# Kernel tuning notes

Hardware: AMD Instinct MI355X
Metric: run time of the kernel (lower is better)

## Reference

```python
import jax, jax.numpy as jnp
import numpy as np

EMB = 1024
HEADS = 16
B, N = 2, 2048

def setup_inputs() -> dict:
    key = jax.random.key(0)
    ks = jax.random.split(key, 9)
    s = 1.0 / np.sqrt(EMB)
    return {
        "x": jax.random.normal(ks[0], (B, N, EMB), dtype=jnp.float32),
        "Wq": jax.random.normal(ks[1], (EMB, EMB), dtype=jnp.float32) * s,
        "bq": jax.random.normal(ks[2], (EMB,), dtype=jnp.float32) * 0.01,
        "Wk": jax.random.normal(ks[3], (EMB, EMB), dtype=jnp.float32) * s,
        "bk": jax.random.normal(ks[4], (EMB,), dtype=jnp.float32) * 0.01,
        "Wv": jax.random.normal(ks[5], (EMB, EMB), dtype=jnp.float32) * s,
        "bv": jax.random.normal(ks[6], (EMB,), dtype=jnp.float32) * 0.01,
        "Wo": jax.random.normal(ks[7], (EMB, EMB), dtype=jnp.float32) * s,
        "bo": jax.random.normal(ks[8], (EMB,), dtype=jnp.float32) * 0.01,
    }

def _split_heads(t):
    b, n, e = t.shape
    return t.reshape(b, n, HEADS, e // HEADS).transpose(0, 2, 1, 3)  # b h n d

def reference(x, Wq, bq, Wk, bk, Wv, bv, Wo, bo):
    q = _split_heads(x @ Wq + bq)
    k = _split_heads(x @ Wk + bk)
    v = _split_heads(x @ Wv + bv)
    # NOTE: original scales by sqrt(emb_size), not sqrt(head_dim)
    scaling = jnp.asarray(EMB, x.dtype) ** 0.5
    energy = jnp.einsum('bhqd,bhkd->bhqk', q, k)
    att = jax.nn.softmax(energy / scaling, axis=-1)
    out = jnp.einsum('bhqk,bhkd->bhqd', att, v)
    out = out.transpose(0, 2, 1, 3).reshape(x.shape[0], x.shape[1], EMB)
    return out @ Wo + bo
```

## Files before the change

kernel.cpp:

```cpp
#include <hip/hip_runtime.h>
#include <hip/hip_bf16.h>

typedef __bf16 bf16_t;
typedef bf16_t bf16x8 __attribute__((ext_vector_type(8)));
typedef float f32x4 __attribute__((ext_vector_type(4)));
typedef float f32x2 __attribute__((ext_vector_type(2)));
typedef float f32x16 __attribute__((ext_vector_type(16)));

#define EMB 1024
#define HEADS 16
#define BATCH 2
#define SEQ 2048
#define HD 64
#define TOKENS (BATCH * SEQ)

__device__ __forceinline__ void gld16(bf16_t* lds_dst, const bf16_t* g_src) {
    __builtin_amdgcn_global_load_lds(
        (const __attribute__((address_space(1))) unsigned int*)g_src,
        (__attribute__((address_space(3))) unsigned int*)lds_dst, 16, 0, 0);
}

__device__ __forceinline__ unsigned cvt_pk_bf16(float lo, float hi) {
    unsigned r;
    asm("v_cvt_pk_bf16_f32 %0, %1, %2" : "=v"(r) : "v"(lo), "v"(hi));
    return r;
}

__device__ __forceinline__ float exp2_fast(float x) {
#if __has_builtin(__builtin_amdgcn_exp2f)
    return __builtin_amdgcn_exp2f(x);
#else
    return __expf(x * 0.69314718056f);
#endif
}

#define WAITV(N) asm volatile("s_waitcnt vmcnt(" #N ")" ::: "memory")
#define BAR() __builtin_amdgcn_s_barrier()

__global__ __launch_bounds__(256) void prep_all(
    const float* __restrict__ x, bf16_t* __restrict__ xb,
    const float* __restrict__ W0, const float* __restrict__ W1,
    const float* __restrict__ W2, const float* __restrict__ W3,
    bf16_t* __restrict__ T0, bf16_t* __restrict__ T1,
    bf16_t* __restrict__ T2, bf16_t* __restrict__ T3) {
    __shared__ __align__(16) bf16_t T[64][72];
    if (blockIdx.x < 1024) {
        size_t i = ((size_t)blockIdx.x * 256 + threadIdx.x) * 16;
        f32x4 v0 = *(const f32x4*)&x[i];
        f32x4 v1 = *(const f32x4*)&x[i + 4];
        f32x4 v2 = *(const f32x4*)&x[i + 8];
        f32x4 v3 = *(const f32x4*)&x[i + 12];
        bf16x8 o0, o1;
#pragma unroll
        for (int j = 0; j < 4; ++j) {
            o0[j] = (bf16_t)v0[j]; o0[4 + j] = (bf16_t)v1[j];
            o1[j] = (bf16_t)v2[j]; o1[4 + j] = (bf16_t)v3[j];
        }
        *(bf16x8*)&xb[i] = o0;
        *(bf16x8*)&xb[i + 8] = o1;
        return;
    }
    int t = blockIdx.x - 1024;
    int z = t >> 8, rid = t & 255;
    const float* src = (z == 0) ? W0 : (z == 1) ? W1 : (z == 2) ? W2 : W3;
    bf16_t* dst = (z == 0) ? T0 : (z == 1) ? T1 : (z == 2) ? T2 : T3;
    int k0 = (rid >> 4) * 64, n0 = (rid & 15) * 64;
    int r = threadIdx.x >> 2, c4 = (threadIdx.x & 3) * 16;
    f32x4 v[4];
#pragma unroll
    for (int q = 0; q < 4; ++q)
        v[q] = *(const f32x4*)&src[(size_t)(k0 + r) * 1024 + n0 + c4 + q * 4];
#pragma unroll
    for (int j = 0; j < 16; ++j) T[c4 + j][r] = (bf16_t)v[j >> 2][j & 3];
    __syncthreads();
    bf16x8 o0 = *(const bf16x8*)&T[r][c4];
    bf16x8 o1 = *(const bf16x8*)&T[r][c4 + 8];
    *(bf16x8*)&dst[(size_t)(n0 + r) * 1024 + k0 + c4] = o0;
    *(bf16x8*)&dst[(size_t)(n0 + r) * 1024 + k0 + c4 + 8] = o1;
}

template <typename TO>
__global__ __launch_bounds__(512) void gemm256(
    const bf16_t* __restrict__ A, const bf16_t* __restrict__ W,
    const float* __restrict__ b0, const float* __restrict__ b1, const float* __restrict__ b2,
    TO* __restrict__ o0, TO* __restrict__ o1, TO* __restrict__ o2,
    int md0, int md1, int md2, float sc0, float sc1, float sc2,
    int MP, int CM, int CSH, int NP) {
    __shared__ __align__(16) bf16_t As[3][256 * 64];
    __shared__ __align__(16) bf16_t Bs[3][128 * 64];

    const int tid = threadIdx.x, w = tid >> 6, lane = tid & 63;
    const int quad = lane >> 4, c = lane & 15;
    const int wm = (w >> 1) * 64, wn = (w & 1) * 64;

    const int lin = blockIdx.x;
    const int xc = lin & 7, t = lin >> 3;
    const int mi = MP * (xc & CM) + (t % MP);
    const int ni = NP * (xc >> CSH) + (t / MP);
    const int m0 = mi * 256, n0 = ni * 128;

    const int z = n0 >> 10;
    const float* bias = (z == 0) ? b0 : (z == 1) ? b1 : b2;
    TO* out = (z == 0) ? o0 : (z == 1) ? o1 : o2;
    const int mode = (z == 0) ? md0 : (z == 1) ? md1 : md2;
    const float scale = (z == 0) ? sc0 : (z == 1) ? sc1 : sc2;
    const int nz = n0 & 1023;

    f32x4 acc[4][4];
#pragma unroll
    for (int i = 0; i < 4; ++i)
#pragma unroll
        for (int j = 0; j < 4; ++j) acc[i][j] = (f32x4){0.f, 0.f, 0.f, 0.f};

    const int r8 = lane >> 3, sg = lane & 7;
    const int g8 = (sg ^ r8) * 8;
    const bf16_t* Ag = A + (size_t)m0 * 1024;
    const bf16_t* Bg = W + (size_t)n0 * 1024;
    int gA[4], lA[4], gB[2], lB[2];
#pragma unroll
    for (int s = 0; s < 4; ++s) {
        lA[s] = (w * 32 + s * 8) * 64;
        gA[s] = (w * 32 + s * 8 + r8) * 1024 + g8;
    }
#pragma unroll
    for (int s = 0; s < 2; ++s) {
        lB[s] = (w * 16 + s * 8) * 64;
        gB[s] = (w * 16 + s * 8 + r8) * 1024 + g8;
    }

    const int so = (quad ^ (c & 7)) * 8;
    int rA[4], rB[4];
#pragma unroll
    for (int i = 0; i < 4; ++i) {
        rA[i] = (wm + i * 16 + c) * 64;
        rB[i] = (wn + i * 16 + c) * 64;
    }

#define STAGE(BUF, T)                                                          \
    {                                                                          \
        int kn = (T) * 64;                                                     \
        _Pragma("unroll")                                                      \
        for (int s = 0; s < 4; ++s) gld16(&As[BUF][lA[s]], &Ag[gA[s] + kn]);   \
        _Pragma("unroll")                                                      \
        for (int s = 0; s < 2; ++s) gld16(&Bs[BUF][lB[s]], &Bg[gB[s] + kn]);   \
    }

#define FRAGS(CUR)                                                             \
    {                                                                          \
        _Pragma("unroll")                                                      \
        for (int ks = 0; ks < 2; ++ks) {                                       \
            int sk = so ^ (ks << 5);                                           \
            bf16x8 af[4], bfv[4];                                              \
            _Pragma("unroll")                                                  \
            for (int i = 0; i < 4; ++i)                                        \
                af[i] = *(const bf16x8*)&As[CUR][rA[i] + sk];                  \
            _Pragma("unroll")                                                  \
            for (int i = 0; i < 4; ++i)                                        \
                bfv[i] = *(const bf16x8*)&Bs[CUR][rB[i] + sk];                 \
            __builtin_amdgcn_s_setprio(1);                                     \
            _Pragma("unroll")                                                  \
            for (int mt = 0; mt < 4; ++mt)                                     \
                _Pragma("unroll")                                              \
                for (int nt = 0; nt < 4; ++nt)                                 \
                    acc[mt][nt] = __builtin_amdgcn_mfma_f32_16x16x32_bf16(     \
                        af[mt], bfv[nt], acc[mt][nt], 0, 0, 0);                \
            __builtin_amdgcn_s_setprio(0);                                     \
        }                                                                      \
    }

#define GSTEP(T, CUR)                                                          \
    {                                                                          \
        WAITV(6);                                                              \
        BAR();                                                                 \
        STAGE(((CUR) + 2) % 3, (T) + 2)                                        \
        FRAGS(CUR)                                                             \
    }

    STAGE(0, 0)
    STAGE(1, 1)
    for (int T = 0; T < 12; T += 3) {
        GSTEP(T, 0)
        GSTEP(T + 1, 1)
        GSTEP(T + 2, 2)
    }
    GSTEP(12, 0)
    GSTEP(13, 1)
    WAITV(6); BAR(); FRAGS(2)
    WAITV(0); BAR(); FRAGS(0)
#undef GSTEP
#undef FRAGS
#undef STAGE

    typedef TO TOx4 __attribute__((ext_vector_type(4)));
#pragma unroll
    for (int nt = 0; nt < 4; ++nt) {
        int colz = nz + wn + nt * 16 + c;
        float bv = bias[colz];
#pragma unroll
        for (int mt = 0; mt < 4; ++mt) {
            if (mode == 2) {
                int row = m0 + wm + mt * 16 + quad * 4;
                int bb = row >> 11, n = row & 2047;
                int hh = colz >> 6, d = colz & 63;
                TOx4 pk;
#pragma unroll
                for (int r = 0; r < 4; ++r)
                    pk[r] = (TO)((acc[mt][nt][r] + bv) * scale);
                *(TOx4*)&out[((size_t)(bb * HEADS + hh) * HD + d) * SEQ + n] = pk;
            } else {
#pragma unroll
                for (int r = 0; r < 4; ++r) {
                    int row = m0 + wm + mt * 16 + quad * 4 + r;
                    float v = (acc[mt][nt][r] + bv) * scale;
                    size_t idx;
                    if (mode == 0) {
                        idx = (size_t)row * 1024 + colz;
                    } else {
                        int bb = row >> 11, n = row & 2047;
                        int hh = colz >> 6, d = colz & 63;
                        idx = ((size_t)(bb * HEADS + hh) * SEQ + n) * HD + d;
                    }
                    out[idx] = (TO)v;
                }
            }
        }
    }
}

__global__ __launch_bounds__(256) void attn_kernel(
    const bf16_t* __restrict__ Q, const bf16_t* __restrict__ K,
    const bf16_t* __restrict__ Vt, bf16_t* __restrict__ O) {
    __shared__ __align__(16) bf16_t Ks[3][64 * 64];
    __shared__ __align__(16) bf16_t Vs[3][64 * 64];

    const int tid = threadIdx.x, w = tid >> 6, lane = tid & 63;
    const int hi = lane >> 5, lq = lane & 31;

    const int lin = blockIdx.x + (blockIdx.y << 4);
    const int xcd = lin & 7, slot = lin >> 3;
    const int bh = xcd + ((slot >> 4) << 3);
    const int q0 = (slot & 15) << 7;
    const int b = bh >> 4, h = bh & 15;

    const int srow8 = lane >> 3, sch = lane & 7;

    const bf16_t* Kg0 = K + (size_t)bh * SEQ * HD;
    const bf16_t* Vg0 = Vt + (size_t)bh * HD * SEQ;

    int sl[2], sgK[2], sgV[2];
#pragma unroll
    for (int s = 0; s < 2; ++s) {
        int rg = (w * 2 + s) * 8;
        int row = rg + srow8;
        int g = sch ^ (row & 7);
        sl[s] = rg * 64;
        sgK[s] = row * 64 + g * 8;
        sgV[s] = row * SEQ + g * 8;
    }
    int rd[4];
#pragma unroll
    for (int dc = 0; dc < 4; ++dc)
        rd[dc] = lq * 64 + (((dc * 2 + hi) ^ (lq & 7)) * 8);

    bf16x8 qf[4];
    {
        const bf16_t* Qrow = Q + ((size_t)bh * SEQ + q0 + w * 32 + lq) * HD;
#pragma unroll
        for (int dc = 0; dc < 4; ++dc)
            qf[dc] = *(const bf16x8*)&Qrow[(dc * 2 + hi) * 8];
    }

#pragma unroll
    for (int s = 0; s < 2; ++s) {
        gld16(&Ks[0][sl[s]], &Kg0[sgK[s]]);
        gld16(&Vs[0][sl[s]], &Vg0[sgV[s]]);
    }
#pragma unroll
    for (int s = 0; s < 2; ++s) {
        gld16(&Ks[1][sl[s]], &Kg0[64 * HD + sgK[s]]);
        gld16(&Vs[1][sl[s]], &Vg0[64 + sgV[s]]);
    }

    f32x16 Zf;
#pragma unroll
    for (int r = 0; r < 16; ++r) Zf[r] = 0.f;

    f32x16 Oacc0, Oacc1;
#pragma unroll
    for (int r = 0; r < 16; ++r) { Oacc0[r] = 0.f; Oacc1[r] = 0.f; }
    f32x2 lpA = (f32x2){0.f, 0.f}, lpB = (f32x2){0.f, 0.f};

    const bf16_t* KgN = Kg0 + 2 * 64 * HD;
    const bf16_t* VgN = Vg0 + 2 * 64;

#define PACKFRAG(SS, c2, dstIdx)                                               \
        {                                                                      \
            unsigned pa = cvt_pk_bf16(SS[8 * (c2) + 0], SS[8 * (c2) + 1]);     \
            unsigned pb = cvt_pk_bf16(SS[8 * (c2) + 4], SS[8 * (c2) + 5]);     \
            unsigned pc = cvt_pk_bf16(SS[8 * (c2) + 2], SS[8 * (c2) + 3]);     \
            unsigned pd = cvt_pk_bf16(SS[8 * (c2) + 6], SS[8 * (c2) + 7]);     \
            asm volatile("v_permlane32_swap_b32 %0, %1" : "+v"(pa), "+v"(pb)); \
            asm volatile("v_permlane32_swap_b32 %0, %1" : "+v"(pc), "+v"(pd)); \
            union { unsigned u[4]; bf16x8 v; } pu;                             \
            pu.u[0] = pa; pu.u[1] = pc; pu.u[2] = pb; pu.u[3] = pd;            \
            pf[dstIdx] = pu.v;                                                 \
        }

#define ACORE(CUR)                                                             \
    {                                                                          \
        f32x16 St0, St1;                                                       \
        __builtin_amdgcn_s_setprio(1);                                         \
        {                                                                      \
            bf16x8 k0 = *(const bf16x8*)&Ks[CUR][rd[0]];                       \
            bf16x8 k1 = *(const bf16x8*)&Ks[CUR][rd[0] + 2048];                \
            St0 = __builtin_amdgcn_mfma_f32_32x32x16_bf16(k0, qf[0], Zf, 0, 0, 0); \
            St1 = __builtin_amdgcn_mfma_f32_32x32x16_bf16(k1, qf[0], Zf, 0, 0, 0); \
        }                                                                      \
        _Pragma("unroll")                                                      \
        for (int dc = 1; dc < 4; ++dc) {                                       \
            bf16x8 k0 = *(const bf16x8*)&Ks[CUR][rd[dc]];                      \
            bf16x8 k1 = *(const bf16x8*)&Ks[CUR][rd[dc] + 2048];               \
            St0 = __builtin_amdgcn_mfma_f32_32x32x16_bf16(k0, qf[dc], St0, 0, 0, 0); \
            St1 = __builtin_amdgcn_mfma_f32_32x32x16_bf16(k1, qf[dc], St1, 0, 0, 0); \
        }                                                                      \
        __builtin_amdgcn_s_setprio(0);                                         \
        _Pragma("unroll")                                                      \
        for (int r = 0; r < 16; r += 2) {                                      \
            St0[r] = exp2_fast(St0[r]); St0[r + 1] = exp2_fast(St0[r + 1]);    \
            lpA += (f32x2){St0[r], St0[r + 1]};                                \
            St1[r] = exp2_fast(St1[r]); St1[r + 1] = exp2_fast(St1[r + 1]);    \
            lpB += (f32x2){St1[r], St1[r + 1]};                                \
        }                                                                      \
        bf16x8 pf[4];                                                          \
        PACKFRAG(St0, 0, 0) PACKFRAG(St0, 1, 1)                                \
        PACKFRAG(St1, 0, 2) PACKFRAG(St1, 1, 3)                                \
        __builtin_amdgcn_s_setprio(1);                                         \
        _Pragma("unroll")                                                      \
        for (int f = 0; f < 4; ++f) {                                          \
            bf16x8 v0 = *(const bf16x8*)&Vs[CUR][rd[f]];                       \
            bf16x8 v1 = *(const bf16x8*)&Vs[CUR][rd[f] + 2048];                \
            Oacc0 = __builtin_amdgcn_mfma_f32_32x32x16_bf16(pf[f], v0, Oacc0, 0, 0, 0); \
            Oacc1 = __builtin_amdgcn_mfma_f32_32x32x16_bf16(pf[f], v1, Oacc1, 0, 0, 0); \
        }                                                                      \
        __builtin_amdgcn_s_setprio(0);                                         \
    }

#define ASTEP(CUR)                                                             \
    {                                                                          \
        WAITV(4);                                                              \
        BAR();                                                                 \
        _Pragma("unroll")                                                      \
        for (int s = 0; s < 2; ++s) {                                          \
            gld16(&Ks[((CUR) + 2) % 3][sl[s]], &KgN[sgK[s]]);                  \
            gld16(&Vs[((CUR) + 2) % 3][sl[s]], &VgN[sgV[s]]);                  \
        }                                                                      \
        KgN += 64 * HD; VgN += 64;                                             \
        ACORE(CUR)                                                             \
    }

    for (int t = 0; t < 30; t += 3) {
        ASTEP(0) ASTEP(1) ASTEP(2)
    }
    WAITV(4); BAR(); ACORE(0)
    WAITV(0); BAR(); ACORE(1)
#undef ASTEP
#undef ACORE
#undef PACKFRAG

    float lp = (lpA[0] + lpA[1]) + (lpB[0] + lpB[1]);
    lp += __shfl_xor(lp, 32);
    float rl = 1.0f / lp;

#pragma unroll
    for (int r = 0; r < 16; ++r) {
        int q_loc = (r & 3) + 8 * (r >> 2) + 4 * hi;
        float rr = __shfl(rl, q_loc);
        int qrow = q0 + w * 32 + q_loc;
        size_t base = ((size_t)(b * SEQ + qrow)) * EMB + h * 64;
        O[base + lq] = (bf16_t)(Oacc0[r] * rr);
        O[base + 32 + lq] = (bf16_t)(Oacc1[r] * rr);
    }
}

extern "C" void kernel_launch(void* const* d_in, const int* in_sizes, int n_in,
                              void* d_out, int out_size, void* d_ws, size_t ws_size,
                              hipStream_t stream) {
    (void)in_sizes; (void)n_in; (void)out_size; (void)ws_size;
    const float* x  = (const float*)d_in[0];
    const float* Wq = (const float*)d_in[1];
    const float* bq = (const float*)d_in[2];
    const float* Wk = (const float*)d_in[3];
    const float* bk = (const float*)d_in[4];
    const float* Wv = (const float*)d_in[5];
    const float* bv = (const float*)d_in[6];
    const float* Wo = (const float*)d_in[7];
    const float* bo = (const float*)d_in[8];

    bf16_t* ws = (bf16_t*)d_ws;
    const size_t NELEM = (size_t)TOKENS * EMB;
    const size_t WELEM = (size_t)EMB * EMB;
    bf16_t* Qb  = ws;
    bf16_t* Kb  = ws + NELEM;
    bf16_t* Vtb = ws + 2 * NELEM;
    bf16_t* Ob  = ws + 3 * NELEM;
    bf16_t* xb  = ws + 4 * NELEM;
    bf16_t* Wt0 = ws + 5 * NELEM;
    bf16_t* Wt1 = Wt0 + WELEM;
    bf16_t* Wt2 = Wt0 + 2 * WELEM;
    bf16_t* Wt3 = Wt0 + 3 * WELEM;
    (void)Wt1; (void)Wt2;

    hipLaunchKernelGGL(prep_all, dim3(2048), dim3(256), 0, stream,
                       x, xb, Wq, Wk, Wv, Wo, Wt0, Wt1, Wt2, Wt3);
    hipLaunchKernelGGL((gemm256<bf16_t>), dim3(384), dim3(512), 0, stream,
                       xb, Wt0, bq, bk, bv, Qb, Kb, Vtb,
                       1, 1, 2, 0.0450842204f, 1.0f, 1.0f,
                       4, 3, 2, 12);
    hipLaunchKernelGGL(attn_kernel, dim3(16, 32), dim3(256), 0, stream, Qb, Kb, Vtb, Ob);
    hipLaunchKernelGGL((gemm256<float>), dim3(128), dim3(512), 0, stream,
                       Ob, Wt3, bo, bo, bo,
                       (float*)d_out, (float*)d_out, (float*)d_out,
                       0, 0, 0, 1.0f, 1.0f, 1.0f,
                       2, 7, 3, 8);
}
```

Measured before the change: 202.7 us.

## Process 128-key tiles per step with double-buffered LDS in attention

The attention loop now handles two 64-key subtiles per iteration (128 keys) using double buffering instead of a 3-stage ring of 64-key tiles. This halves the number of barriers and waits per key and gives more independent MFMAs per phase, and launch bounds now request 2 blocks per SM. The cost is a shallower prefetch (one tile ahead, with a full wait vmcnt(0) before each barrier) and higher register pressure from four score accumulators and eight P fragments.

Result: faster. 198.0 us (-2.3%).

```diff
diff --git a/kernel.cpp b/kernel.cpp
--- a/kernel.cpp
+++ b/kernel.cpp
@@ -227,11 +227,11 @@
     }
 }
 
-__global__ __launch_bounds__(256) void attn_kernel(
+__global__ __launch_bounds__(256, 2) void attn_kernel(
     const bf16_t* __restrict__ Q, const bf16_t* __restrict__ K,
     const bf16_t* __restrict__ Vt, bf16_t* __restrict__ O) {
-    __shared__ __align__(16) bf16_t Ks[3][64 * 64];
-    __shared__ __align__(16) bf16_t Vs[3][64 * 64];
+    __shared__ __align__(16) bf16_t Ks[2][2 * 64 * 64];
+    __shared__ __align__(16) bf16_t Vs[2][2 * 64 * 64];
 
     const int tid = threadIdx.x, w = tid >> 6, lane = tid & 63;
     const int hi = lane >> 5, lq = lane & 31;
@@ -270,16 +270,20 @@
             qf[dc] = *(const bf16x8*)&Qrow[(dc * 2 + hi) * 8];
     }
 
-#pragma unroll
-    for (int s = 0; s < 2; ++s) {
-        gld16(&Ks[0][sl[s]], &Kg0[sgK[s]]);
-        gld16(&Vs[0][sl[s]], &Vg0[sgV[s]]);
-    }
-#pragma unroll
-    for (int s = 0; s < 2; ++s) {
-        gld16(&Ks[1][sl[s]], &Kg0[64 * HD + sgK[s]]);
-        gld16(&Vs[1][sl[s]], &Vg0[64 + sgV[s]]);
-    }
+#define STAGEPH(BUF, PH)                                                       \
+    {                                                                          \
+        const bf16_t* Kp = Kg0 + (size_t)(PH) * 128 * HD;                      \
+        const bf16_t* Vp = Vg0 + (PH) * 128;                                   \
+        _Pragma("unroll")                                                      \
+        for (int s = 0; s < 2; ++s) {                                          \
+            gld16(&Ks[BUF][sl[s]], &Kp[sgK[s]]);                               \
+            gld16(&Ks[BUF][4096 + sl[s]], &Kp[4096 + sgK[s]]);                 \
+            gld16(&Vs[BUF][sl[s]], &Vp[sgV[s]]);                               \
+            gld16(&Vs[BUF][4096 + sl[s]], &Vp[64 + sgV[s]]);                   \
+        }                                                                      \
+    }
+
+    STAGEPH(0, 0)
 
     f32x16 Zf;
 #pragma unroll
@@ -289,9 +293,6 @@
 #pragma unroll
     for (int r = 0; r < 16; ++r) { Oacc0[r] = 0.f; Oacc1[r] = 0.f; }
     f32x2 lpA = (f32x2){0.f, 0.f}, lpB = (f32x2){0.f, 0.f};
-
-    const bf16_t* KgN = Kg0 + 2 * 64 * HD;
-    const bf16_t* VgN = Vg0 + 2 * 64;
 
 #define PACKFRAG(SS, c2, dstIdx)                                               \
         {                                                                      \
@@ -306,66 +307,79 @@
             pf[dstIdx] = pu.v;                                                 \
         }
 
-#define ACORE(CUR)                                                             \
+#define MFMA32(A, B, C) __builtin_amdgcn_mfma_f32_32x32x16_bf16(A, B, C, 0, 0, 0)
+
+#define ACORE2(BUF)                                                            \
     {                                                                          \
-        f32x16 St0, St1;                                                       \
+        f32x16 SA0, SA1, SB0, SB1;                                             \
         __builtin_amdgcn_s_setprio(1);                                         \
         {                                                                      \
-            bf16x8 k0 = *(const bf16x8*)&Ks[CUR][rd[0]];                       \
-            bf16x8 k1 = *(const bf16x8*)&Ks[CUR][rd[0] + 2048];                \
-            St0 = __builtin_amdgcn_mfma_f32_32x32x16_bf16(k0, qf[0], Zf, 0, 0, 0); \
-            St1 = __builtin_amdgcn_mfma_f32_32x32x16_bf16(k1, qf[0], Zf, 0, 0, 0); \
+            bf16x8 a0 = *(const bf16x8*)&Ks[BUF][rd[0]];                       \
+            bf16x8 a1 = *(const bf16x8*)&Ks[BUF][rd[0] + 2048];                \
+            bf16x8 b0 = *(const bf16x8*)&Ks[BUF][rd[0] + 4096];                \
+            bf16x8 b1 = *(const bf16x8*)&Ks[BUF][rd[0] + 6144];                \
+            SA0 = MFMA32(a0, qf[0], Zf);                                       \
+            SA1 = MFMA32(a1, qf[0], Zf);                                       \
+            SB0 = MFMA32(b0, qf[0], Zf);                                       \
+            SB1 = MFMA32(b1, qf[0], Zf);                                       \
         }                                                                      \
         _Pragma("unroll")                                                      \
         for (int dc = 1; dc < 4; ++dc) {                                       \
-            bf16x8 k0 = *(const bf16x8*)&Ks[CUR][rd[dc]];                      \
-            bf16x8 k1 = *(const bf16x8*)&Ks[CUR][rd[dc] + 2048];               \
-            St0 = __builtin_amdgcn_mfma_f32_32x32x16_bf16(k0, qf[dc], St0, 0, 0, 0); \
-            St1 = __builtin_amdgcn_mfma_f32_32x32x16_bf16(k1, qf[dc], St1, 0, 0, 0); \
+            bf16x8 a0 = *(const bf16x8*)&Ks[BUF][rd[dc]];                      \
+            bf16x8 a1 = *(const bf16x8*)&Ks[BUF][rd[dc] + 2048];               \
+            bf16x8 b0 = *(const bf16x8*)&Ks[BUF][rd[dc] + 4096];               \
+            bf16x8 b1 = *(const bf16x8*)&Ks[BUF][rd[dc] + 6144];               \
+            SA0 = MFMA32(a0, qf[dc], SA0);                                     \
+            SA1 = MFMA32(a1, qf[dc], SA1);                                     \
+            SB0 = MFMA32(b0, qf[dc], SB0);                                     \
+            SB1 = MFMA32(b1, qf[dc], SB1);                                     \
         }                                                                      \
         __builtin_amdgcn_s_setprio(0);                                         \
         _Pragma("unroll")                                                      \
         for (int r = 0; r < 16; r += 2) {                                      \
-            St0[r] = exp2_fast(St0[r]); St0[r + 1] = exp2_fast(St0[r + 1]);    \
-            lpA += (f32x2){St0[r], St0[r + 1]};                                \
-            St1[r] = exp2_fast(St1[r]); St1[r + 1] = exp2_fast(St1[r + 1]);    \
-            lpB += (f32x2){St1[r], St1[r + 1]};                                \
-        }                                                                      \
-        bf16x8 pf[4];                                                          \
-        PACKFRAG(St0, 0, 0) PACKFRAG(St0, 1, 1)                                \
-        PACKFRAG(St1, 0, 2) PACKFRAG(St1, 1, 3)                                \
+            SA0[r] = exp2_fast(SA0[r]); SA0[r + 1] = exp2_fast(SA0[r + 1]);    \
+            lpA += (f32x2){SA0[r], SA0[r + 1]};                                \
+            SA1[r] = exp2_fast(SA1[r]); SA1[r + 1] = exp2_fast(SA1[r + 1]);    \
+            lpB += (f32x2){SA1[r], SA1[r + 1]};                                \
+            SB0[r] = exp2_fast(SB0[r]); SB0[r + 1] = exp2_fast(SB0[r + 1]);    \
+            lpA += (f32x2){SB0[r], SB0[r + 1]};                                \
+            SB1[r] = exp2_fast(SB1[r]); SB1[r + 1] = exp2_fast(SB1[r + 1]);    \
+            lpB += (f32x2){SB1[r], SB1[r + 1]};                                \
+        }                                                                      \
+        bf16x8 pf[8];                                                          \
+        PACKFRAG(SA0, 0, 0) PACKFRAG(SA0, 1, 1)                                \
+        PACKFRAG(SA1, 0, 2) PACKFRAG(SA1, 1, 3)                                \
+        PACKFRAG(SB0, 0, 4) PACKFRAG(SB0, 1, 5)                                \
+        PACKFRAG(SB1, 0, 6) PACKFRAG(SB1, 1, 7)                                \
         __builtin_amdgcn_s_setprio(1);                                         \
         _Pragma("unroll")                                                      \
         for (int f = 0; f < 4; ++f) {                                          \
-            bf16x8 v0 = *(const bf16x8*)&Vs[CUR][rd[f]];                       \
-            bf16x8 v1 = *(const bf16x8*)&Vs[CUR][rd[f] + 2048];                \
-            Oacc0 = __builtin_amdgcn_mfma_f32_32x32x16_bf16(pf[f], v0, Oacc0, 0, 0, 0); \
-            Oacc1 = __builtin_amdgcn_mfma_f32_32x32x16_bf16(pf[f], v1, Oacc1, 0, 0, 0); \
+            bf16x8 vA0 = *(const bf16x8*)&Vs[BUF][rd[f]];                      \
+            bf16x8 vA1 = *(const bf16x8*)&Vs[BUF][rd[f] + 2048];               \
+            bf16x8 vB0 = *(const bf16x8*)&Vs[BUF][rd[f] + 4096];               \
+            bf16x8 vB1 = *(const bf16x8*)&Vs[BUF][rd[f] + 6144];               \
+            Oacc0 = MFMA32(pf[f], vA0, Oacc0);                                 \
+            Oacc1 = MFMA32(pf[f], vA1, Oacc1);                                 \
+            Oacc0 = MFMA32(pf[4 + f], vB0, Oacc0);                             \
+            Oacc1 = MFMA32(pf[4 + f], vB1, Oacc1);                             \
         }                                                                      \
         __builtin_amdgcn_s_setprio(0);                                         \
     }
 
-#define ASTEP(CUR)                                                             \
-    {                                                                          \
-        WAITV(4);                                                              \
-        BAR();                                                                 \
-        _Pragma("unroll")                                                      \
-        for (int s = 0; s < 2; ++s) {                                          \
-            gld16(&Ks[((CUR) + 2) % 3][sl[s]], &KgN[sgK[s]]);                  \
-            gld16(&Vs[((CUR) + 2) % 3][sl[s]], &VgN[sgV[s]]);                  \
-        }                                                                      \
-        KgN += 64 * HD; VgN += 64;                                             \
-        ACORE(CUR)                                                             \
-    }
-
-    for (int t = 0; t < 30; t += 3) {
-        ASTEP(0) ASTEP(1) ASTEP(2)
-    }
-    WAITV(4); BAR(); ACORE(0)
-    WAITV(0); BAR(); ACORE(1)
-#undef ASTEP
-#undef ACORE
+    for (int p = 0; p < 16; p += 2) {
+        WAITV(0);
+        BAR();
+        STAGEPH(1, p + 1)
+        ACORE2(0)
+        WAITV(0);
+        BAR();
+        if (p < 14) STAGEPH(0, p + 2)
+        ACORE2(1)
+    }
+#undef ACORE2
+#undef MFMA32
 #undef PACKFRAG
+#undef STAGEPH
 
     float lp = (lpA[0] + lpA[1]) + (lpB[0] + lpB[1]);
     lp += __shfl_xor(lp, 32);
```
